# Performance work log

Hardware: AMD Instinct MI355X
Metric: run time of the kernel (lower is better)

## Reference

```python
import jax, jax.numpy as jnp
import numpy as np

D_MODEL = 1024
D_HIDDEN = 1024  # must equal D_MODEL (SSM adds C(h) [.,d_model] + D(x) [.,d_hidden])
B, T = 8, 1022   # T chosen so T+2 == D_MODEL, required by the `x @ x_res` batched matmul


def setup_inputs() -> dict:
    key = jax.random.key(0)
    ks = jax.random.split(key, 12)
    def w(k, shape, s=0.02):
        return jax.random.normal(k, shape, jnp.float32) * s
    return {
        "x": jax.random.normal(ks[0], (B, T, D_MODEL), jnp.float32),
        "w1": w(ks[1], (D_MODEL, D_MODEL)),
        "w2": w(ks[2], (D_MODEL, D_MODEL)),
        "w_last": w(ks[3], (D_MODEL, D_MODEL)),
        "conv_w": w(ks[4], (D_MODEL, 1, 3), 0.1),  # depthwise conv kernel [out, in/groups, k]
        "conv_b": jnp.zeros((D_MODEL,), jnp.float32),
        "A": jnp.abs(jax.random.normal(ks[5], (D_HIDDEN,), jnp.float32)) + 0.1,  # positive -> stable decay
        "wB": w(ks[6], (D_MODEL, D_HIDDEN)), "bB": jnp.zeros((D_HIDDEN,), jnp.float32),
        "wC": w(ks[7], (D_HIDDEN, D_MODEL)), "bC": jnp.zeros((D_MODEL,), jnp.float32),
        "wD": w(ks[8], (D_MODEL, D_HIDDEN)), "bD": jnp.zeros((D_HIDDEN,), jnp.float32),
        "wdelta": w(ks[9], (D_MODEL, D_HIDDEN)), "bdelta": jnp.zeros((D_HIDDEN,), jnp.float32),
    }


def _scan_combine(l, r):
    # linear recurrence h_t = a_t * h_{t-1} + b_t as an associative op
    aL, bL = l
    aR, bR = r
    return (aL * aR, aR * bL + bR)


def reference(x, w1, w2, w_last, conv_w, conv_b, A, wB, bB, wC, bC, wD, bD, wdelta, bdelta):
    x = x @ w1  # [B,T,D]
    # depthwise causal-ish conv, padding=2 on both sides (as in torch code) -> length T+2
    xc = jnp.transpose(x, (0, 2, 1))  # [B,D,T]
    xc = jax.lax.conv_general_dilated(
        xc, conv_w, window_strides=(1,), padding=[(2, 2)],
        dimension_numbers=("NCH", "OIH", "NCH"), feature_group_count=D_MODEL)
    xc = xc + conv_b[None, :, None]
    x = jnp.transpose(xc, (0, 2, 1))  # [B, T+2, D]
    x = jax.nn.silu(x)
    # --- SSM selective scan ---
    x_delta = jax.nn.softplus(x @ wdelta + bdelta)      # [B,T+2,Dh]
    A_bar = jnp.exp(-x_delta * A)                       # [B,T+2,Dh]
    B_x = x @ wB + bB                                   # [B,T+2,Dh]
    _, h = jax.lax.associative_scan(_scan_combine, (A_bar, B_x), axis=1)
    ssm_out = (h @ wC + bC) + (x @ wD + bD)             # [B,T+2,D] (Dh == D)
    # --- gating + output ---
    x_res = jax.nn.silu(ssm_out @ w2)                   # [B,T+2,D]
    z = jnp.matmul(ssm_out, x_res)                      # batched matmul: valid since D == T+2
    out = z @ w_last                                    # [B, T+2, D]
    return out
```

## Files before the change

### kernel.cpp

```cpp
#include <hip/hip_runtime.h>

typedef __bf16 bf16x8 __attribute__((ext_vector_type(8)));
typedef float  f32x4  __attribute__((ext_vector_type(4)));
typedef unsigned short u16x8 __attribute__((ext_vector_type(8)));

__device__ __forceinline__ float b2f(unsigned short u) {
  union { float f; unsigned int i; } v; v.i = ((unsigned int)u) << 16; return v.f;
}
__device__ __forceinline__ unsigned short f2b(float f) {
  union { float f; unsigned int i; } v; v.f = f;
  unsigned int r = v.i + 0x7fffu + ((v.i >> 16) & 1u);
  return (unsigned short)(r >> 16);
}

__device__ __forceinline__ void async_copy16(const unsigned short* g, unsigned short* l) {
  __builtin_amdgcn_global_load_lds(
      (__attribute__((address_space(1))) void*)g,
      (__attribute__((address_space(3))) void*)l, 16, 0, 0);
}

__global__ void k_prep(const float* w0, const float* w1_, const float* w2_,
                       const float* w3_, const float* w4_, const float* w5_,
                       const float* w6_, unsigned short* dst,
                       const float* cw, float* cwT,
                       const float* x, unsigned short* xb) {
  const int tx = threadIdx.x, ty = threadIdx.y;
  const int z = blockIdx.z;
  if (z >= 8) {
    const int fb = (z - 8) * 1024 + blockIdx.y * 32 + blockIdx.x;
    const size_t i = ((size_t)(fb * 256 + ty * 32 + tx)) << 2;
    const int d = (int)(i & 1023);
    const int row = (int)(i >> 10);
    const int t = row & 1023, b = row >> 10;
    float4 v = make_float4(0.f, 0.f, 0.f, 0.f);
    if (t < 1022) v = *(const float4*)&x[((size_t)(b * 1022 + t) << 10) + d];
    ushort4 o;
    o.x = f2b(v.x); o.y = f2b(v.y); o.z = f2b(v.z); o.w = f2b(v.w);
    *(ushort4*)&xb[i] = o;
    return;
  }
  if (z == 7) {
    const int flat = (blockIdx.y * 32 + blockIdx.x) * 256 + ty * 32 + tx;
    if (flat < 3072) {
      const int d = flat & 1023, j = flat >> 10;
      cwT[flat] = cw[d * 3 + j];
    }
    return;
  }
  const float* srcs[7] = {w0, w1_, w2_, w3_, w4_, w5_, w6_};
  const float* src = srcs[z];
  unsigned short* d = dst + ((size_t)z << 20);
  __shared__ float tile[32][33];
  const int bn = blockIdx.x << 5, bk = blockIdx.y << 5;
#pragma unroll
  for (int i = 0; i < 4; ++i)
    tile[ty + i * 8][tx] = src[(size_t)(bk + ty + i * 8) * 1024 + bn + tx];
  __syncthreads();
#pragma unroll
  for (int i = 0; i < 4; ++i)
    d[(size_t)(bn + ty + i * 8) * 1024 + bk + tx] = f2b(tile[tx][ty + i * 8]);
}

__global__ void k_conv_silu(const unsigned short* __restrict__ x1, const float* __restrict__ cwT,
                            const float* __restrict__ cb, unsigned short* __restrict__ xs) {
  const int gid = blockIdx.x * 256 + threadIdx.x;
  const int pair = gid >> 7;
  const int d0 = (gid & 127) << 3;
  const int b = pair >> 9, t0 = (pair & 511) << 1;
  float w[3][8];
#pragma unroll
  for (int j = 0; j < 3; ++j) {
    float4 a = *(const float4*)&cwT[j * 1024 + d0];
    float4 c = *(const float4*)&cwT[j * 1024 + d0 + 4];
    w[j][0] = a.x; w[j][1] = a.y; w[j][2] = a.z; w[j][3] = a.w;
    w[j][4] = c.x; w[j][5] = c.y; w[j][6] = c.z; w[j][7] = c.w;
  }
  float base[8];
  {
    float4 c0 = *(const float4*)&cb[d0], c1 = *(const float4*)&cb[d0 + 4];
    base[0] = c0.x; base[1] = c0.y; base[2] = c0.z; base[3] = c0.w;
    base[4] = c1.x; base[5] = c1.y; base[6] = c1.z; base[7] = c1.w;
  }
  float rv[4][8];
#pragma unroll
  for (int r = 0; r < 4; ++r) {
    const int t = t0 + r - 2;
    if (t >= 0) {
      u16x8 v = *(const u16x8*)&x1[((size_t)(b * 1024 + t) << 10) + d0];
#pragma unroll
      for (int k = 0; k < 8; ++k) rv[r][k] = b2f(v[k]);
    } else {
#pragma unroll
      for (int k = 0; k < 8; ++k) rv[r][k] = 0.f;
    }
  }
  u16x8 o0, o1;
#pragma unroll
  for (int k = 0; k < 8; ++k) {
    float a0 = base[k] + rv[0][k] * w[0][k] + rv[1][k] * w[1][k] + rv[2][k] * w[2][k];
    float a1 = base[k] + rv[1][k] * w[0][k] + rv[2][k] * w[1][k] + rv[3][k] * w[2][k];
    o0[k] = f2b(a0 / (1.f + __expf(-a0)));
    o1[k] = f2b(a1 / (1.f + __expf(-a1)));
  }
  *(u16x8*)&xs[((size_t)(b * 1024 + t0) << 10) + d0] = o0;
  *(u16x8*)&xs[((size_t)(b * 1024 + t0 + 1) << 10) + d0] = o1;
}

__global__ void k_scan1(const unsigned short* __restrict__ y, const unsigned short* __restrict__ Bx,
                        float* __restrict__ cA, float* __restrict__ cB) {
  const int g = blockIdx.x * 256 + threadIdx.x;
  const int d = g & 1023, bc = g >> 10;
  const int b = bc >> 4, c = bc & 15;
  size_t base = ((size_t)(b * 1024 + c * 64) << 10) + d;
  float aA = 1.f, aB = 0.f;
  for (int t = 0; t < 64; ++t) {
    float a = __expf(-b2f(y[base]));
    float bx = b2f(Bx[base]);
    aA *= a; aB = a * aB + bx; base += 1024;
  }
  cA[g] = aA; cB[g] = aB;
}
__global__ void k_scan2(const float* __restrict__ cA, const float* __restrict__ cB,
                        float* __restrict__ carry) {
  const int g = blockIdx.x * 256 + threadIdx.x;
  const int d = g & 1023, b = g >> 10;
  float a[16], bb[16];
#pragma unroll
  for (int c = 0; c < 16; ++c) {
    const int idx = ((b * 16 + c) << 10) + d;
    a[c] = cA[idx]; bb[c] = cB[idx];
  }
  float sB = 0.f;
#pragma unroll
  for (int c = 0; c < 16; ++c) {
    carry[((b * 16 + c) << 10) + d] = sB;
    sB = a[c] * sB + bb[c];
  }
}
__global__ void k_scan3(const unsigned short* __restrict__ y, const unsigned short* __restrict__ Bx,
                        const float* __restrict__ carry, unsigned short* __restrict__ hb) {
  const int g = blockIdx.x * 256 + threadIdx.x;
  const int d = g & 1023, bc = g >> 10;
  const int b = bc >> 4, c = bc & 15;
  size_t base = ((size_t)(b * 1024 + c * 64) << 10) + d;
  float h = carry[g];
  for (int t = 0; t < 64; ++t) {
    float a = __expf(-b2f(y[base]));
    float bx = b2f(Bx[base]);
    h = a * h + bx;
    hb[base] = f2b(h);
    base += 1024;
  }
}

__global__ void k_transpose_xres(const unsigned short* __restrict__ src,
                                 unsigned short* __restrict__ dst) {
  __shared__ unsigned short tile[32][33];
  const int b = blockIdx.z;
  const int bx = blockIdx.x << 5, by = blockIdx.y << 5;
  const int tx = threadIdx.x, ty = threadIdx.y;
  const unsigned short* s = src + ((size_t)b << 20);
  unsigned short* d = dst + ((size_t)b << 20);
#pragma unroll
  for (int i = 0; i < 4; ++i)
    tile[ty + i * 8][tx] = s[(size_t)(by + ty + i * 8) * 1024 + bx + tx];
  __syncthreads();
#pragma unroll
  for (int i = 0; i < 4; ++i)
    d[(size_t)(bx + ty + i * 8) * 1024 + by + tx] = tile[tx][ty + i * 8];
}

template <int EPI, bool BATCHB>
__global__ __launch_bounds__(256)
void k_gemm(const unsigned short* __restrict__ A, const unsigned short* __restrict__ Bt,
            void* __restrict__ outp, const float* __restrict__ aux1,
            const void* __restrict__ aux2) {
  __shared__ unsigned short As[2][128 * 64];
  __shared__ unsigned short Bs[2][128 * 64];
  const int tid = threadIdx.x;

  const int nxb = gridDim.x;
  const int nwg = nxb * gridDim.y;
  int lin = blockIdx.y * nxb + blockIdx.x;
  lin = (lin & 7) * (nwg >> 3) + (lin >> 3);
  const int CH = nxb << 3;
  const int grp = lin / CH, idx = lin % CH;
  const int m0 = ((grp << 3) + (idx & 7)) << 7;
  const int n0 = (idx >> 3) << 7;

  const int wid = tid >> 6, l = tid & 63;
  const int wr = ((wid >> 1) << 6);
  const int wc = ((wid & 1) << 6);
  const int lr = l & 15, kg = l >> 4;
  const unsigned short* Bp = BATCHB ? Bt + ((size_t)(m0 >> 10) << 20) : Bt;

  f32x4 acc[4][4];
#pragma unroll
  for (int i = 0; i < 4; ++i)
#pragma unroll
    for (int j = 0; j < 4; ++j) acc[i][j] = (f32x4){0.f, 0.f, 0.f, 0.f};

  const int frow = tid >> 3;
  const int fchunk = (tid & 7) ^ (frow & 7);
  const unsigned short* ga[4];
  const unsigned short* gb[4];
#pragma unroll
  for (int it = 0; it < 4; ++it) {
    ga[it] = A  + (size_t)(m0 + frow + it * 32) * 1024 + (fchunk << 3);
    gb[it] = Bp + (size_t)(n0 + frow + it * 32) * 1024 + (fchunk << 3);
  }

#define STAGE(buf)                                                              \
  {                                                                             \
    _Pragma("unroll")                                                           \
    for (int it = 0; it < 4; ++it)                                              \
      async_copy16(ga[it], &As[buf][(tid << 3) + it * 2048]);                   \
    _Pragma("unroll")                                                           \
    for (int it = 0; it < 4; ++it)                                              \
      async_copy16(gb[it], &Bs[buf][(tid << 3) + it * 2048]);                   \
    _Pragma("unroll")                                                           \
    for (int it = 0; it < 4; ++it) { ga[it] += 64; gb[it] += 64; }              \
  }

  const int c0 = kg ^ (lr & 7);
  const int aOff0 = ((wr + lr) << 7) + (c0 << 4);
  const int aOff1 = aOff0 ^ 64;
  const int bOff0 = ((wc + lr) << 7) + (c0 << 4);
  const int bOff1 = bOff0 ^ 64;
  const char* AsB = (const char*)&As[0][0];
  const char* BsB = (const char*)&Bs[0][0];

  STAGE(0);
  STAGE(1);

#pragma unroll
  for (int t = 0; t < 16; ++t) {
    const int cur = t & 1;
    if (t < 15) asm volatile("s_waitcnt vmcnt(8)" ::: "memory");
    else        asm volatile("s_waitcnt vmcnt(0)" ::: "memory");
    __builtin_amdgcn_s_barrier();
    __builtin_amdgcn_sched_barrier(0);
    __builtin_amdgcn_s_setprio(1);
    const char* pa = AsB + (cur << 14);
    const char* pb = BsB + (cur << 14);
    {
      bf16x8 aF[4], bF[4];
#pragma unroll
      for (int mi = 0; mi < 4; ++mi) aF[mi] = *(const bf16x8*)(pa + aOff0 + mi * 2048);
#pragma unroll
      for (int ni = 0; ni < 4; ++ni) bF[ni] = *(const bf16x8*)(pb + bOff0 + ni * 2048);
#pragma unroll
      for (int mi = 0; mi < 4; ++mi)
#pragma unroll
        for (int ni = 0; ni < 4; ++ni)
          acc[mi][ni] = __builtin_amdgcn_mfma_f32_16x16x32_bf16(bF[ni], aF[mi], acc[mi][ni], 0, 0, 0);
    }
    {
      bf16x8 aF[4], bF[4];
#pragma unroll
      for (int mi = 0; mi < 4; ++mi) aF[mi] = *(const bf16x8*)(pa + aOff1 + mi * 2048);
#pragma unroll
      for (int ni = 0; ni < 4; ++ni) bF[ni] = *(const bf16x8*)(pb + bOff1 + ni * 2048);
#pragma unroll
      for (int mi = 0; mi < 4; ++mi)
#pragma unroll
        for (int ni = 0; ni < 4; ++ni)
          acc[mi][ni] = __builtin_amdgcn_mfma_f32_16x16x32_bf16(bF[ni], aF[mi], acc[mi][ni], 0, 0, 0);
    }
    __builtin_amdgcn_s_setprio(0);
    asm volatile("s_waitcnt lgkmcnt(0)" ::: "memory");
    __builtin_amdgcn_s_barrier();
    __builtin_amdgcn_sched_barrier(0);
    if (t + 2 < 16) STAGE(cur);
  }
#undef STAGE

#pragma unroll
  for (int mi = 0; mi < 4; ++mi) {
    const int row = m0 + wr + mi * 16 + lr;
    const size_t rbase = (size_t)row << 10;
#pragma unroll
    for (int ni = 0; ni < 4; ++ni) {
      const int colb = n0 + wc + ni * 16 + (kg << 2);
      const f32x4 v = acc[mi][ni];
      if (EPI == 0) {
        ushort4 o; o.x = f2b(v[0]); o.y = f2b(v[1]); o.z = f2b(v[2]); o.w = f2b(v[3]);
        *(ushort4*)&((unsigned short*)outp)[rbase + colb] = o;
      } else if (EPI == 2) {
        const float4 b4 = *(const float4*)&aux1[colb];
        ushort4 o;
        o.x = f2b(v[0] + b4.x); o.y = f2b(v[1] + b4.y);
        o.z = f2b(v[2] + b4.z); o.w = f2b(v[3] + b4.w);
        *(ushort4*)&((unsigned short*)outp)[rbase + colb] = o;
      } else if (EPI == 3) {
        const float4 b4 = *(const float4*)&aux1[colb];
        const ushort4 xv = *(const ushort4*)&((const unsigned short*)aux2)[rbase + colb];
        ushort4 o;
        o.x = f2b(v[0] + b4.x + b2f(xv.x)); o.y = f2b(v[1] + b4.y + b2f(xv.y));
        o.z = f2b(v[2] + b4.z + b2f(xv.z)); o.w = f2b(v[3] + b4.w + b2f(xv.w));
        *(ushort4*)&((unsigned short*)outp)[rbase + colb] = o;
      } else if (EPI == 4) {
        ushort4 o;
        o.x = f2b(v[0] / (1.f + __expf(-v[0]))); o.y = f2b(v[1] / (1.f + __expf(-v[1])));
        o.z = f2b(v[2] / (1.f + __expf(-v[2]))); o.w = f2b(v[3] / (1.f + __expf(-v[3])));
        *(ushort4*)&((unsigned short*)outp)[rbase + colb] = o;
      } else if (EPI == 5) {
        float4 o; o.x = v[0]; o.y = v[1]; o.z = v[2]; o.w = v[3];
        *(float4*)&((float*)outp)[rbase + colb] = o;
      } else {
        const float4 b4 = *(const float4*)&aux1[colb];
        const float4 a4 = *(const float4*)&((const float*)aux2)[colb];
        ushort4 o;
        float t0 = v[0] + b4.x; float sp = (t0 > 15.f) ? t0 : __logf(1.f + __expf(t0));
        o.x = f2b(sp * a4.x);
        float t1 = v[1] + b4.y; sp = (t1 > 15.f) ? t1 : __logf(1.f + __expf(t1));
        o.y = f2b(sp * a4.y);
        float t2 = v[2] + b4.z; sp = (t2 > 15.f) ? t2 : __logf(1.f + __expf(t2));
        o.z = f2b(sp * a4.z);
        float t3 = v[3] + b4.w; sp = (t3 > 15.f) ? t3 : __logf(1.f + __expf(t3));
        o.w = f2b(sp * a4.w);
        *(ushort4*)&((unsigned short*)outp)[rbase + colb] = o;
      }
    }
  }
}

extern "C" void kernel_launch(void* const* d_in, const int* in_sizes, int n_in,
                              void* d_out, int out_size, void* d_ws, size_t ws_size,
                              hipStream_t stream) {
  const float* x      = (const float*)d_in[0];
  const float* w1     = (const float*)d_in[1];
  const float* w2     = (const float*)d_in[2];
  const float* w_last = (const float*)d_in[3];
  const float* conv_w = (const float*)d_in[4];
  const float* conv_b = (const float*)d_in[5];
  const float* Avec   = (const float*)d_in[6];
  const float* wB     = (const float*)d_in[7];
  const float* bB     = (const float*)d_in[8];
  const float* wC     = (const float*)d_in[9];
  const float* bC     = (const float*)d_in[10];
  const float* wD     = (const float*)d_in[11];
  const float* bD     = (const float*)d_in[12];
  const float* wdelta = (const float*)d_in[13];
  const float* bdelta = (const float*)d_in[14];

  char* ws = (char*)d_ws;
  const size_t MB = 1ull << 20;
  const size_t NW = 1ull << 20;
  unsigned short* wT   = (unsigned short*)(ws);
  unsigned short* xb   = (unsigned short*)(ws + 14 * MB);
  unsigned short* x1   = (unsigned short*)(ws + 30 * MB);
  unsigned short* xs   = (unsigned short*)(ws + 46 * MB);
  unsigned short* y    = (unsigned short*)(ws + 62 * MB);
  unsigned short* z    = (unsigned short*)(ws + 78 * MB);
  unsigned short* Bx   = (unsigned short*)(ws + 94 * MB);
  unsigned short* xD   = (unsigned short*)(ws + 110 * MB);
  float*          cA   = (float*)(ws + 126 * MB);
  float*          cB   = (float*)(ws + 126 * MB + 512 * 1024);
  float*          carry= (float*)(ws + 127 * MB);
  float*          cwT  = (float*)(ws + 127 * MB + 512 * 1024);
  unsigned short* hb    = xs;
  unsigned short* ssm   = xb;
  unsigned short* xres  = x1;
  unsigned short* xresT = y;

  dim3 bT(32, 8);
  dim3 gG(8, 64);

  k_prep<<<dim3(32, 32, 16), bT, 0, stream>>>(w1, wdelta, wB, wD, wC, w2, w_last, wT,
                                              conv_w, cwT, x, xb);
  k_gemm<0, false><<<gG, 256, 0, stream>>>(xb, wT + 0 * NW, x1, nullptr, nullptr);
  k_conv_silu<<<2048, 256, 0, stream>>>(x1, cwT, conv_b, xs);
  k_gemm<6, false><<<gG, 256, 0, stream>>>(xs, wT + 1 * NW, y, bdelta, (const void*)Avec);
  k_gemm<2, false><<<gG, 256, 0, stream>>>(xs, wT + 2 * NW, Bx, bB, nullptr);
  k_gemm<2, false><<<gG, 256, 0, stream>>>(xs, wT + 3 * NW, xD, bD, nullptr);
  k_scan1<<<512, 256, 0, stream>>>(y, Bx, cA, cB);
  k_scan2<<<32, 256, 0, stream>>>(cA, cB, carry);
  k_scan3<<<512, 256, 0, stream>>>(y, Bx, carry, hb);
  k_gemm<3, false><<<gG, 256, 0, stream>>>(hb, wT + 4 * NW, ssm, bC, (const void*)xD);
  k_gemm<4, false><<<gG, 256, 0, stream>>>(ssm, wT + 5 * NW, xres, nullptr, nullptr);
  k_transpose_xres<<<dim3(32, 32, 8), bT, 0, stream>>>(xres, xresT);
  k_gemm<0, true><<<gG, 256, 0, stream>>>(ssm, xresT, z, nullptr, nullptr);
  k_gemm<5, false><<<gG, 256, 0, stream>>>(z, wT + 6 * NW, (float*)d_out, nullptr, nullptr);
}
```

Measured before the change: 245.8 us.

## Fuse xres transpose into GEMM epilogue and merge scan carry pass

The silu(ssm@w2) GEMM now writes its tile through swizzled LDS and stores it transposed, which removes the separate transpose kernel and its extra round trip through global memory. The scan's carry-propagation kernel is folded into the final scan pass: each chunk recomputes its prefix from the chunk summaries. Both scan kernels now handle two channels per thread with 32-bit loads and stores. The costs are redundant carry work of up to 15 steps per chunk, fewer threads in the scan kernels, and extra LDS traffic plus a barrier in the GEMM epilogue.

```diff
diff --git a/kernel.cpp b/kernel.cpp
--- a/kernel.cpp
+++ b/kernel.cpp
@@ -108,66 +108,51 @@
 
 __global__ void k_scan1(const unsigned short* __restrict__ y, const unsigned short* __restrict__ Bx,
                         float* __restrict__ cA, float* __restrict__ cB) {
-  const int g = blockIdx.x * 256 + threadIdx.x;
-  const int d = g & 1023, bc = g >> 10;
+  const int p = blockIdx.x * 256 + threadIdx.x;
+  const int d2 = p & 511, bc = p >> 9;
   const int b = bc >> 4, c = bc & 15;
-  size_t base = ((size_t)(b * 1024 + c * 64) << 10) + d;
-  float aA = 1.f, aB = 0.f;
+  const int d0 = d2 << 1;
+  size_t base = ((size_t)(b * 1024 + c * 64) << 10) + d0;
+  float aA0 = 1.f, aB0 = 0.f, aA1 = 1.f, aB1 = 0.f;
   for (int t = 0; t < 64; ++t) {
-    float a = __expf(-b2f(y[base]));
-    float bx = b2f(Bx[base]);
-    aA *= a; aB = a * aB + bx; base += 1024;
-  }
-  cA[g] = aA; cB[g] = aB;
-}
-__global__ void k_scan2(const float* __restrict__ cA, const float* __restrict__ cB,
-                        float* __restrict__ carry) {
-  const int g = blockIdx.x * 256 + threadIdx.x;
-  const int d = g & 1023, b = g >> 10;
-  float a[16], bb[16];
-#pragma unroll
-  for (int c = 0; c < 16; ++c) {
-    const int idx = ((b * 16 + c) << 10) + d;
-    a[c] = cA[idx]; bb[c] = cB[idx];
-  }
-  float sB = 0.f;
-#pragma unroll
-  for (int c = 0; c < 16; ++c) {
-    carry[((b * 16 + c) << 10) + d] = sB;
-    sB = a[c] * sB + bb[c];
-  }
-}
-__global__ void k_scan3(const unsigned short* __restrict__ y, const unsigned short* __restrict__ Bx,
-                        const float* __restrict__ carry, unsigned short* __restrict__ hb) {
-  const int g = blockIdx.x * 256 + threadIdx.x;
-  const int d = g & 1023, bc = g >> 10;
+    const unsigned int yy = *(const unsigned int*)&y[base];
+    const unsigned int bb = *(const unsigned int*)&Bx[base];
+    const float a0 = __expf(-b2f((unsigned short)yy));
+    const float a1 = __expf(-b2f((unsigned short)(yy >> 16)));
+    aA0 *= a0; aB0 = a0 * aB0 + b2f((unsigned short)bb);
+    aA1 *= a1; aB1 = a1 * aB1 + b2f((unsigned short)(bb >> 16));
+    base += 1024;
+  }
+  const int gi = (bc << 10) + d0;
+  *(float2*)&cA[gi] = make_float2(aA0, aA1);
+  *(float2*)&cB[gi] = make_float2(aB0, aB1);
+}
+__global__ void k_scan23(const unsigned short* __restrict__ y, const unsigned short* __restrict__ Bx,
+                         const float* __restrict__ cA, const float* __restrict__ cB,
+                         unsigned short* __restrict__ hb) {
+  const int p = blockIdx.x * 256 + threadIdx.x;
+  const int d2 = p & 511, bc = p >> 9;
   const int b = bc >> 4, c = bc & 15;
-  size_t base = ((size_t)(b * 1024 + c * 64) << 10) + d;
-  float h = carry[g];
+  const int d0 = d2 << 1;
+  float h0 = 0.f, h1 = 0.f;
+  for (int cp = 0; cp < c; ++cp) {
+    const int gi = (((b << 4) + cp) << 10) + d0;
+    const float2 a = *(const float2*)&cA[gi];
+    const float2 bb = *(const float2*)&cB[gi];
+    h0 = a.x * h0 + bb.x;
+    h1 = a.y * h1 + bb.y;
+  }
+  size_t base = ((size_t)(b * 1024 + c * 64) << 10) + d0;
   for (int t = 0; t < 64; ++t) {
-    float a = __expf(-b2f(y[base]));
-    float bx = b2f(Bx[base]);
-    h = a * h + bx;
-    hb[base] = f2b(h);
+    const unsigned int yy = *(const unsigned int*)&y[base];
+    const unsigned int bb = *(const unsigned int*)&Bx[base];
+    const float a0 = __expf(-b2f((unsigned short)yy));
+    const float a1 = __expf(-b2f((unsigned short)(yy >> 16)));
+    h0 = a0 * h0 + b2f((unsigned short)bb);
+    h1 = a1 * h1 + b2f((unsigned short)(bb >> 16));
+    *(unsigned int*)&hb[base] = (unsigned int)f2b(h0) | ((unsigned int)f2b(h1) << 16);
     base += 1024;
   }
-}
-
-__global__ void k_transpose_xres(const unsigned short* __restrict__ src,
-                                 unsigned short* __restrict__ dst) {
-  __shared__ unsigned short tile[32][33];
-  const int b = blockIdx.z;
-  const int bx = blockIdx.x << 5, by = blockIdx.y << 5;
-  const int tx = threadIdx.x, ty = threadIdx.y;
-  const unsigned short* s = src + ((size_t)b << 20);
-  unsigned short* d = dst + ((size_t)b << 20);
-#pragma unroll
-  for (int i = 0; i < 4; ++i)
-    tile[ty + i * 8][tx] = s[(size_t)(by + ty + i * 8) * 1024 + bx + tx];
-  __syncthreads();
-#pragma unroll
-  for (int i = 0; i < 4; ++i)
-    d[(size_t)(bx + ty + i * 8) * 1024 + by + tx] = tile[tx][ty + i * 8];
 }
 
 template <int EPI, bool BATCHB>
@@ -274,6 +259,43 @@
     if (t + 2 < 16) STAGE(cur);
   }
 #undef STAGE
+
+  if (EPI == 7) {
+    char* ltb = (char*)&As[0][0];
+#pragma unroll
+    for (int mi = 0; mi < 4; ++mi) {
+      const int rl = wr + mi * 16 + lr;
+      const int sw = (((rl & 7) ^ ((rl >> 3) & 7)) << 4);
+#pragma unroll
+      for (int ni = 0; ni < 4; ++ni) {
+        const int cl = wc + ni * 16 + (kg << 2);
+        const f32x4 v = acc[mi][ni];
+        ushort4 o;
+        o.x = f2b(v[0] / (1.f + __expf(-v[0]))); o.y = f2b(v[1] / (1.f + __expf(-v[1])));
+        o.z = f2b(v[2] / (1.f + __expf(-v[2]))); o.w = f2b(v[3] / (1.f + __expf(-v[3])));
+        *(ushort4*)(ltb + (((rl << 8) + (cl << 1)) ^ sw)) = o;
+      }
+    }
+    __syncthreads();
+    const int bb = m0 >> 10;
+    const int tbase = m0 & 1023;
+    unsigned short* dstT = (unsigned short*)outp + ((size_t)bb << 20);
+#pragma unroll
+    for (int it = 0; it < 8; ++it) {
+      const int flat = tid + it * 256;
+      const int dl = flat >> 4;
+      const int tl = (flat & 15) << 3;
+      u16x8 o;
+#pragma unroll
+      for (int j = 0; j < 8; ++j) {
+        const int r = tl + j;
+        const int sw = (((r & 7) ^ ((r >> 3) & 7)) << 4);
+        o[j] = *(const unsigned short*)(ltb + (((r << 8) + (dl << 1)) ^ sw));
+      }
+      *(u16x8*)&dstT[(size_t)(n0 + dl) * 1024 + tbase + tl] = o;
+    }
+    return;
+  }
 
 #pragma unroll
   for (int mi = 0; mi < 4; ++mi) {
@@ -299,11 +321,6 @@
         o.x = f2b(v[0] + b4.x + b2f(xv.x)); o.y = f2b(v[1] + b4.y + b2f(xv.y));
         o.z = f2b(v[2] + b4.z + b2f(xv.z)); o.w = f2b(v[3] + b4.w + b2f(xv.w));
         *(ushort4*)&((unsigned short*)outp)[rbase + colb] = o;
-      } else if (EPI == 4) {
-        ushort4 o;
-        o.x = f2b(v[0] / (1.f + __expf(-v[0]))); o.y = f2b(v[1] / (1.f + __expf(-v[1])));
-        o.z = f2b(v[2] / (1.f + __expf(-v[2]))); o.w = f2b(v[3] / (1.f + __expf(-v[3])));
-        *(ushort4*)&((unsigned short*)outp)[rbase + colb] = o;
       } else if (EPI == 5) {
         float4 o; o.x = v[0]; o.y = v[1]; o.z = v[2]; o.w = v[3];
         *(float4*)&((float*)outp)[rbase + colb] = o;
@@ -357,11 +374,9 @@
   unsigned short* xD   = (unsigned short*)(ws + 110 * MB);
   float*          cA   = (float*)(ws + 126 * MB);
   float*          cB   = (float*)(ws + 126 * MB + 512 * 1024);
-  float*          carry= (float*)(ws + 127 * MB);
-  float*          cwT  = (float*)(ws + 127 * MB + 512 * 1024);
+  float*          cwT  = (float*)(ws + 127 * MB);
   unsigned short* hb    = xs;
   unsigned short* ssm   = xb;
-  unsigned short* xres  = x1;
   unsigned short* xresT = y;
 
   dim3 bT(32, 8);
@@ -374,12 +389,10 @@
   k_gemm<6, false><<<gG, 256, 0, stream>>>(xs, wT + 1 * NW, y, bdelta, (const void*)Avec);
   k_gemm<2, false><<<gG, 256, 0, stream>>>(xs, wT + 2 * NW, Bx, bB, nullptr);
   k_gemm<2, false><<<gG, 256, 0, stream>>>(xs, wT + 3 * NW, xD, bD, nullptr);
-  k_scan1<<<512, 256, 0, stream>>>(y, Bx, cA, cB);
-  k_scan2<<<32, 256, 0, stream>>>(cA, cB, carry);
-  k_scan3<<<512, 256, 0, stream>>>(y, Bx, carry, hb);
+  k_scan1<<<256, 256, 0, stream>>>(y, Bx, cA, cB);
+  k_scan23<<<256, 256, 0, stream>>>(y, Bx, cA, cB, hb);
   k_gemm<3, false><<<gG, 256, 0, stream>>>(hb, wT + 4 * NW, ssm, bC, (const void*)xD);
-  k_gemm<4, false><<<gG, 256, 0, stream>>>(ssm, wT + 5 * NW, xres, nullptr, nullptr);
-  k_transpose_xres<<<dim3(32, 32, 8), bT, 0, stream>>>(xres, xresT);
+  k_gemm<7, false><<<gG, 256, 0, stream>>>(ssm, wT + 5 * NW, xresT, nullptr, nullptr);
   k_gemm<0, true><<<gG, 256, 0, stream>>>(ssm, xresT, z, nullptr, nullptr);
   k_gemm<5, false><<<gG, 256, 0, stream>>>(z, wT + 6 * NW, (float*)d_out, nullptr, nullptr);
 }
```

After: 241.2 us. No clear change (-1.9%).
